# Kernel optimization log

Hardware: AMD Instinct MI355X
Metric: run time of the kernel (lower is better)

## Reference

```python
import jax, jax.numpy as jnp
import numpy as np

N = 8192
E = 262144
NFEAT = 200
NHID = 128
NOUT = 16
CLUSTERS = (10, 5)


def _layernorm(x, g, b, eps=1e-5):
    mu = jnp.mean(x, axis=-1, keepdims=True)
    var = jnp.var(x, axis=-1, keepdims=True)
    return (x - mu) / jnp.sqrt(var + eps) * g + b


def _gumbel_softmax_hard(logits, g, tau=1.0):
    # straight-through gumbel softmax (hard=True), dim=1
    y = jax.nn.softmax((logits + g) / tau, axis=1)
    hard = jax.nn.one_hot(jnp.argmax(y, axis=1), y.shape[1], dtype=y.dtype)
    return hard + y - jax.lax.stop_gradient(y)


def _row_normalize(x, eps=1e-12):
    n = jnp.linalg.norm(x, axis=1, keepdims=True)
    return x / jnp.maximum(n, eps)


def setup_inputs() -> dict:
    key = jax.random.key(0)
    ks = jax.random.split(key, 20)
    u0 = jax.random.uniform(ks[3], (N, CLUSTERS[0]), minval=1e-6, maxval=1.0 - 1e-6)
    u1 = jax.random.uniform(ks[4], (CLUSTERS[0], CLUSTERS[1]), minval=1e-6, maxval=1.0 - 1e-6)
    s = 0.05
    return {
        'x': jax.random.normal(ks[0], (N, NFEAT), dtype=jnp.float32),
        'edge_index': jax.random.randint(ks[1], (2, E), 0, N, dtype=jnp.int32),
        'edge_weight': jax.random.uniform(ks[2], (E,), dtype=jnp.float32),
        'gumbel0': -jnp.log(-jnp.log(u0)),
        'gumbel1': -jnp.log(-jnp.log(u1)),
        # GCN params (2 layers, layernorm)
        'Wg1': jax.random.normal(ks[5], (NHID, NFEAT)) * s,
        'bg1': jnp.zeros((NHID,)),
        'ln1_g': jnp.ones((NHID,)), 'ln1_b': jnp.zeros((NHID,)),
        'Wg2': jax.random.normal(ks[6], (NHID, NHID)) * s,
        'bg2': jnp.zeros((NHID,)),
        'ln2_g': jnp.ones((NHID,)), 'ln2_b': jnp.zeros((NHID,)),
        # per-level pool + encoder linears
        'pool0_W': jax.random.normal(ks[7], (CLUSTERS[0], NHID)) * s,
        'pool0_b': jnp.zeros((CLUSTERS[0],)),
        'pool1_W': jax.random.normal(ks[8], (CLUSTERS[1], NHID)) * s,
        'pool1_b': jnp.zeros((CLUSTERS[1],)),
        'enc0_W': jax.random.normal(ks[9], (NHID, NHID)) * s,
        'enc0_b': jnp.zeros((NHID,)),
        'enc1_W': jax.random.normal(ks[10], (NHID, NHID)) * s,
        'enc1_b': jnp.zeros((NHID,)),
        'fc_W': jax.random.normal(ks[11], (NOUT, 3 * NHID)) * s,
        'fc_b': jnp.zeros((NOUT,)),
    }


def reference(x, edge_index, edge_weight, gumbel0, gumbel1,
              Wg1, bg1, ln1_g, ln1_b, Wg2, bg2, ln2_g, ln2_b,
              pool0_W, pool0_b, pool1_W, pool1_b,
              enc0_W, enc0_b, enc1_W, enc1_b, fc_W, fc_b):
    src, dst = edge_index[0], edge_index[1]

    def agg(h):  # weighted neighbor sum: out[i] = sum_{e: dst_e=i} w_e * h[src_e]
        return jax.ops.segment_sum(h[src] * edge_weight[:, None], dst, num_segments=N)

    # bottom GCN encoder (2 layers, layernorm)
    h = agg(x) @ Wg1.T + bg1
    h = jax.nn.relu(_layernorm(h, ln1_g, ln1_b))
    h = agg(h) @ Wg2.T + bg2
    h = _layernorm(h, ln2_g, ln2_b)
    latent = jax.nn.relu(h)  # [N, nhid]
    all_latents = [latent]

    # dense adjacency (to_dense_adj)
    adj = jnp.zeros((N, N), dtype=x.dtype).at[src, dst].add(edge_weight)

    pools = [(pool0_W, pool0_b), (pool1_W, pool1_b)]
    encs = [(enc0_W, enc0_b), (enc1_W, enc1_b)]
    gumbels = [gumbel0, gumbel1]
    product = None
    for level in range(len(CLUSTERS)):
        pW, pb = pools[level]
        eW, eb = encs[level]
        assign = _gumbel_softmax_hard(latent @ pW.T + pb, gumbels[level])  # [n_l, K]
        product = assign if level == 0 else product @ assign  # [N, K]
        xc = _row_normalize(assign.T @ latent)  # [K, nhid]
        adj = assign.T @ adj @ assign  # [K, K]
        adj = adj / jnp.sum(adj + 1e-8)
        latent = jax.nn.relu((adj @ xc) @ eW.T + eb)  # [K, nhid]
        all_latents.append(product @ latent)  # [N, nhid]

    rep = jnp.concatenate(all_latents, axis=1)  # [N, 3*nhid]
    return rep @ fc_W.T + fc_b
```

## Files before the change

### kernel.cpp

```cpp
#include <hip/hip_runtime.h>

#define N_NODES 8192
#define N_EDGES 262144
#define NFEAT 200
#define NHID 128

template<int K>
__device__ __forceinline__ void gemm_body(const float* __restrict__ A,
                                          const float* __restrict__ W,
                                          float* __restrict__ C, int bid) {
    __shared__ float a_s[8 * K];
    int row0 = bid * 8;
    const float* Ab = A + (size_t)row0 * K;
    for (int idx = threadIdx.x; idx < 8 * K; idx += 128) a_s[idx] = Ab[idx];
    __syncthreads();
    int j = threadIdx.x;
    float acc[8] = {0.f, 0.f, 0.f, 0.f, 0.f, 0.f, 0.f, 0.f};
    const float4* W4 = (const float4*)(W + (size_t)j * K);
    for (int k4 = 0; k4 < K / 4; ++k4) {
        float4 w = W4[k4];
        int k = k4 * 4;
        #pragma unroll
        for (int r = 0; r < 8; ++r) {
            const float* ar = a_s + r * K + k;
            acc[r] += ar[0] * w.x + ar[1] * w.y + ar[2] * w.z + ar[3] * w.w;
        }
    }
    #pragma unroll
    for (int r = 0; r < 8; ++r) C[(size_t)(row0 + r) * 128 + j] = acc[r];
}

template<int K>
__global__ __launch_bounds__(128) void gemm_rows(const float* __restrict__ A,
                                                 const float* __restrict__ W,
                                                 float* __restrict__ C) {
    gemm_body<K>(A, W, C, blockIdx.x);
}

__global__ __launch_bounds__(128) void gemm1_hist(const float* __restrict__ A,
                                                  const float* __restrict__ W,
                                                  float* __restrict__ C,
                                                  const int* __restrict__ ei,
                                                  int* __restrict__ deg) {
    if (blockIdx.x < N_NODES / 8) {
        gemm_body<NFEAT>(A, W, C, blockIdx.x);
    } else {
        const int* dst = ei + N_EDGES;
        for (int e = (blockIdx.x - N_NODES / 8) * 128 + threadIdx.x; e < N_EDGES; e += 64 * 128)
            atomicAdd(&deg[dst[e]], 1);
    }
}

__global__ __launch_bounds__(256) void scan_kernel(const int* __restrict__ deg,
                                                   int* __restrict__ row_start,
                                                   int* __restrict__ cursor) {
    __shared__ int part[256];
    __shared__ int partx[257];
    int tid = threadIdx.x;
    int base = tid * 32;
    int s = 0;
    for (int i = 0; i < 32; ++i) s += deg[base + i];
    part[tid] = s;
    __syncthreads();
    if (tid == 0) {
        int run = 0;
        for (int i = 0; i < 256; ++i) { partx[i] = run; run += part[i]; }
        partx[256] = run;
    }
    __syncthreads();
    int run = partx[tid];
    for (int i = 0; i < 32; ++i) {
        row_start[base + i] = run;
        cursor[base + i] = run;
        run += deg[base + i];
    }
    if (tid == 255) row_start[N_NODES] = run;
}

__global__ __launch_bounds__(256) void scatter_kernel(const int* __restrict__ ei,
                                                      const float* __restrict__ ew,
                                                      int* __restrict__ cursor,
                                                      int2* __restrict__ esort, int E) {
    int e = blockIdx.x * blockDim.x + threadIdx.x;
    if (e < E) {
        int d = ei[E + e];
        int pos = atomicAdd(&cursor[d], 1);
        esort[pos] = make_int2(ei[e], __float_as_int(ew[e]));
    }
}

__global__ __launch_bounds__(256) void agg_ln_csr(const int* __restrict__ row_start,
                                                  const int2* __restrict__ esort,
                                                  const float* __restrict__ H,
                                                  float* __restrict__ out,
                                                  const float* __restrict__ bias,
                                                  const float* __restrict__ g,
                                                  const float* __restrict__ b) {
    int wave = (blockIdx.x * blockDim.x + threadIdx.x) >> 6;
    int lane = threadIdx.x & 63;
    int s0 = row_start[wave], s1 = row_start[wave + 1];
    float ax0 = 0.f, ay0 = 0.f, ax1 = 0.f, ay1 = 0.f;
    float ax2 = 0.f, ay2 = 0.f, ax3 = 0.f, ay3 = 0.f;
    int e = s0;
    for (; e + 3 < s1; e += 4) {
        int2 p0 = esort[e], p1 = esort[e + 1], p2 = esort[e + 2], p3 = esort[e + 3];
        float2 v0 = *(const float2*)(H + (size_t)p0.x * 128 + lane * 2);
        float2 v1 = *(const float2*)(H + (size_t)p1.x * 128 + lane * 2);
        float2 v2 = *(const float2*)(H + (size_t)p2.x * 128 + lane * 2);
        float2 v3 = *(const float2*)(H + (size_t)p3.x * 128 + lane * 2);
        float w0 = __int_as_float(p0.y), w1 = __int_as_float(p1.y);
        float w2 = __int_as_float(p2.y), w3 = __int_as_float(p3.y);
        ax0 += w0 * v0.x; ay0 += w0 * v0.y;
        ax1 += w1 * v1.x; ay1 += w1 * v1.y;
        ax2 += w2 * v2.x; ay2 += w2 * v2.y;
        ax3 += w3 * v3.x; ay3 += w3 * v3.y;
    }
    for (; e < s1; ++e) {
        int2 p0 = esort[e];
        float2 v0 = *(const float2*)(H + (size_t)p0.x * 128 + lane * 2);
        float w0 = __int_as_float(p0.y);
        ax0 += w0 * v0.x; ay0 += w0 * v0.y;
    }
    float2 bs = *(const float2*)(bias + lane * 2);
    float vx = (ax0 + ax1) + (ax2 + ax3) + bs.x;
    float vy = (ay0 + ay1) + (ay2 + ay3) + bs.y;
    float s = vx + vy;
    float ss = vx * vx + vy * vy;
    for (int off = 32; off; off >>= 1) {
        s += __shfl_xor(s, off, 64);
        ss += __shfl_xor(ss, off, 64);
    }
    float mu = s * (1.f / 128.f);
    float var = ss * (1.f / 128.f) - mu * mu;
    float rs = rsqrtf(var + 1e-5f);
    float2 gg = *(const float2*)(g + lane * 2);
    float2 bb = *(const float2*)(b + lane * 2);
    float y0 = fmaxf((vx - mu) * rs * gg.x + bb.x, 0.f);
    float y1 = fmaxf((vy - mu) * rs * gg.y + bb.y, 0.f);
    *(float2*)(out + (size_t)wave * 128 + lane * 2) = make_float2(y0, y1);
}

__global__ __launch_bounds__(256) void pool0_xc0(const float* __restrict__ latent,
                                                 const float* __restrict__ pW,
                                                 const float* __restrict__ pb,
                                                 const float* __restrict__ gum,
                                                 int* __restrict__ c0,
                                                 float* __restrict__ partials) {
    __shared__ float Ws[10 * 128];
    __shared__ float bs[10];
    __shared__ float acc[1280];
    for (int i = threadIdx.x; i < 1280; i += 256) { Ws[i] = pW[i]; acc[i] = 0.f; }
    if (threadIdx.x < 10) bs[threadIdx.x] = pb[threadIdx.x];
    __syncthreads();
    int lane = threadIdx.x & 63;
    int sub = lane & 7;
    int row = blockIdx.x * 32 + (threadIdx.x >> 6) * 8 + (lane >> 3);

    const float4* lp = (const float4*)(latent + (size_t)row * 128 + sub * 16);
    float4 x0 = lp[0], x1 = lp[1], x2 = lp[2], x3 = lp[3];
    float2 gj[5];
    #pragma unroll
    for (int j = 0; j < 5; ++j) gj[j] = *(const float2*)(gum + (size_t)row * 10 + j * 2);

    float p[10];
    #pragma unroll
    for (int k = 0; k < 10; ++k) {
        const float4* wk = (const float4*)(Ws + k * 128 + sub * 16);
        float4 w0 = wk[0], w1 = wk[1], w2 = wk[2], w3 = wk[3];
        float a = x0.x * w0.x + x0.y * w0.y + x0.z * w0.z + x0.w * w0.w;
        a += x1.x * w1.x + x1.y * w1.y + x1.z * w1.z + x1.w * w1.w;
        a += x2.x * w2.x + x2.y * w2.y + x2.z * w2.z + x2.w * w2.w;
        a += x3.x * w3.x + x3.y * w3.y + x3.z * w3.z + x3.w * w3.w;
        p[k] = a;
    }
    #pragma unroll
    for (int off = 1; off < 8; off <<= 1) {
        #pragma unroll
        for (int k = 0; k < 10; ++k) p[k] += __shfl_xor(p[k], off, 64);
    }
    int best = 0;
    float bv = p[0] + bs[0] + gj[0].x;
    #pragma unroll
    for (int k = 1; k < 10; ++k) {
        float gk = (k & 1) ? gj[k >> 1].y : gj[k >> 1].x;
        float z = p[k] + bs[k] + gk;
        if (z > bv) { bv = z; best = k; }
    }
    if (sub == 0) c0[row] = best;
    float* ap = acc + best * 128 + sub * 16;
    atomicAdd(ap + 0, x0.x);  atomicAdd(ap + 1, x0.y);
    atomicAdd(ap + 2, x0.z);  atomicAdd(ap + 3, x0.w);
    atomicAdd(ap + 4, x1.x);  atomicAdd(ap + 5, x1.y);
    atomicAdd(ap + 6, x1.z);  atomicAdd(ap + 7, x1.w);
    atomicAdd(ap + 8, x2.x);  atomicAdd(ap + 9, x2.y);
    atomicAdd(ap + 10, x2.z); atomicAdd(ap + 11, x2.w);
    atomicAdd(ap + 12, x3.x); atomicAdd(ap + 13, x3.y);
    atomicAdd(ap + 14, x3.z); atomicAdd(ap + 15, x3.w);
    __syncthreads();
    for (int i = threadIdx.x; i < 1280; i += 256)
        partials[(size_t)blockIdx.x * 1280 + i] = acc[i];
}

__global__ __launch_bounds__(256) void adj_xc0(const int* __restrict__ ei,
                                               const float* __restrict__ ew,
                                               const int* __restrict__ c0,
                                               float* __restrict__ A0,
                                               const float* __restrict__ partials,
                                               float* __restrict__ xc0, int E) {
    if (blockIdx.x < 256) {
        __shared__ float As[100];
        for (int i = threadIdx.x; i < 100; i += 256) As[i] = 0.f;
        __syncthreads();
        const int* src = ei;
        const int* dst = ei + E;
        for (int e = blockIdx.x * 256 + threadIdx.x; e < E; e += 256 * 256) {
            int a = c0[src[e]], b = c0[dst[e]];
            atomicAdd(&As[a * 10 + b], ew[e]);
        }
        __syncthreads();
        for (int i = threadIdx.x; i < 100; i += 256) atomicAdd(&A0[i], As[i]);
    } else {
        int k = blockIdx.x - 256;
        int d = threadIdx.x & 127;
        int half = threadIdx.x >> 7;
        int b0 = half * 128;
        float s0 = 0.f, s1 = 0.f, s2 = 0.f, s3 = 0.f;
        for (int b = b0; b < b0 + 128; b += 4) {
            s0 += partials[(size_t)(b    ) * 1280 + k * 128 + d];
            s1 += partials[(size_t)(b + 1) * 1280 + k * 128 + d];
            s2 += partials[(size_t)(b + 2) * 1280 + k * 128 + d];
            s3 += partials[(size_t)(b + 3) * 1280 + k * 128 + d];
        }
        __shared__ float sm[256];
        sm[threadIdx.x] = (s0 + s1) + (s2 + s3);
        __syncthreads();
        if (threadIdx.x < 128) xc0[k * 128 + d] = sm[threadIdx.x] + sm[threadIdx.x + 128];
    }
}

__global__ __launch_bounds__(256) void small_kernel(const float* __restrict__ xc0,
                                                    const float* __restrict__ A0,
                                                    const float* __restrict__ gum1,
                                                    const float* __restrict__ p1W,
                                                    const float* __restrict__ p1b,
                                                    const float* __restrict__ e0W,
                                                    const float* __restrict__ e0b,
                                                    const float* __restrict__ e1W,
                                                    const float* __restrict__ e1b,
                                                    const float* __restrict__ fcW,
                                                    const float* __restrict__ fcb,
                                                    float* __restrict__ tbl) {
    __shared__ float xc0n[10 * 128];
    __shared__ float adj0[100];
    __shared__ float m0[10 * 128];
    __shared__ float l1[10 * 128];
    __shared__ float xc1n[5 * 128];
    __shared__ float l2[5 * 128];
    __shared__ float A1[25];
    __shared__ int c1[10];
    __shared__ float red[4];

    int tid = threadIdx.x;
    int wid = tid >> 6, lane = tid & 63;

    for (int r = wid; r < 10; r += 4) {
        float2 v = *(const float2*)(xc0 + r * 128 + lane * 2);
        float ss = v.x * v.x + v.y * v.y;
        for (int off = 32; off; off >>= 1) ss += __shfl_xor(ss, off, 64);
        float sc = 1.f / fmaxf(sqrtf(ss), 1e-12f);
        xc0n[r * 128 + lane * 2] = v.x * sc;
        xc0n[r * 128 + lane * 2 + 1] = v.y * sc;
    }
    __syncthreads();
    if (tid == 0) {
        float s = 0.f;
        for (int i = 0; i < 100; ++i) s += A0[i];
        red[0] = s + 1e-6f;
    }
    __syncthreads();
    if (tid < 100) adj0[tid] = A0[tid] / red[0];
    __syncthreads();
    for (int idx = tid; idx < 1280; idx += 256) {
        int r = idx >> 7, d = idx & 127;
        float acc = 0.f;
        #pragma unroll
        for (int a = 0; a < 10; ++a) acc += adj0[r * 10 + a] * xc0n[a * 128 + d];
        m0[idx] = acc;
    }
    __syncthreads();
    for (int idx = tid; idx < 1280; idx += 256) {
        int r = idx >> 7, d = idx & 127;
        float acc = e0b[d];
        const float* wrow = e0W + d * 128;
        for (int k = 0; k < 128; ++k) acc += m0[r * 128 + k] * wrow[k];
        l1[idx] = fmaxf(acc, 0.f);
    }
    __syncthreads();
    if (tid < 10) {
        int best = 0;
        float bv = -1e30f;
        for (int j = 0; j < 5; ++j) {
            float acc = p1b[j] + gum1[tid * 5 + j];
            const float* wrow = p1W + j * 128;
            for (int k = 0; k < 128; ++k) acc += l1[tid * 128 + k] * wrow[k];
            if (acc > bv) { bv = acc; best = j; }
        }
        c1[tid] = best;
    }
    __syncthreads();
    for (int idx = tid; idx < 640; idx += 256) {
        int m = idx >> 7, d = idx & 127;
        float acc = 0.f;
        #pragma unroll
        for (int k = 0; k < 10; ++k)
            if (c1[k] == m) acc += l1[k * 128 + d];
        xc1n[idx] = acc;
    }
    __syncthreads();
    for (int r = wid; r < 5; r += 4) {
        float2 v = *(const float2*)(xc1n + r * 128 + lane * 2);
        float ss = v.x * v.x + v.y * v.y;
        for (int off = 32; off; off >>= 1) ss += __shfl_xor(ss, off, 64);
        float sc = 1.f / fmaxf(sqrtf(ss), 1e-12f);
        xc1n[r * 128 + lane * 2] = v.x * sc;
        xc1n[r * 128 + lane * 2 + 1] = v.y * sc;
    }
    __syncthreads();
    if (tid < 25) {
        int m = tid / 5, n = tid % 5;
        float acc = 0.f;
        for (int a = 0; a < 10; ++a)
            for (int b = 0; b < 10; ++b)
                if (c1[a] == m && c1[b] == n) acc += adj0[a * 10 + b];
        A1[tid] = acc;
    }
    __syncthreads();
    if (tid == 0) {
        float s = 0.f;
        for (int i = 0; i < 25; ++i) s += A1[i];
        red[1] = s + 25e-8f;
    }
    __syncthreads();
    float den1 = red[1];
    for (int idx = tid; idx < 640; idx += 256) {
        int r = idx >> 7, d = idx & 127;
        float acc = 0.f;
        #pragma unroll
        for (int a = 0; a < 5; ++a) acc += A1[r * 5 + a] * xc1n[a * 128 + d];
        m0[idx] = acc / den1;
    }
    __syncthreads();
    for (int idx = tid; idx < 640; idx += 256) {
        int r = idx >> 7, d = idx & 127;
        float acc = e1b[d];
        const float* wrow = e1W + d * 128;
        for (int k = 0; k < 128; ++k) acc += m0[r * 128 + k] * wrow[k];
        l2[idx] = fmaxf(acc, 0.f);
    }
    __syncthreads();
    for (int idx = tid; idx < 160; idx += 256) {
        int k = idx >> 4, o = idx & 15;
        float acc = fcb[o];
        const float* fB = fcW + o * 384 + 128;
        const float* fC = fcW + o * 384 + 256;
        const float* a1 = l1 + k * 128;
        const float* a2 = l2 + c1[k] * 128;
        for (int d = 0; d < 128; ++d) acc += a1[d] * fB[d] + a2[d] * fC[d];
        tbl[idx] = acc;
    }
}

__global__ __launch_bounds__(256) void out_kernel(const float* __restrict__ latent,
                                                  const int* __restrict__ c0,
                                                  const float* __restrict__ tbl,
                                                  const float* __restrict__ fcW,
                                                  float* __restrict__ out) {
    __shared__ float fA[16 * 128];
    __shared__ float ts[160];
    for (int i = threadIdx.x; i < 2048; i += 256) {
        int o = i >> 7, d = i & 127;
        fA[i] = fcW[o * 384 + d];
    }
    for (int i = threadIdx.x; i < 160; i += 256) ts[i] = tbl[i];
    __syncthreads();
    int lane = threadIdx.x & 63;
    int sub = lane & 7;
    int row = blockIdx.x * 32 + (threadIdx.x >> 6) * 8 + (lane >> 3);
    const float4* lp = (const float4*)(latent + (size_t)row * 128 + sub * 16);
    float4 x0 = lp[0], x1 = lp[1], x2 = lp[2], x3 = lp[3];
    float p[16];
    #pragma unroll
    for (int o = 0; o < 16; ++o) {
        const float4* fo = (const float4*)(fA + o * 128 + sub * 16);
        float4 w0 = fo[0], w1 = fo[1], w2 = fo[2], w3 = fo[3];
        float a = x0.x * w0.x + x0.y * w0.y + x0.z * w0.z + x0.w * w0.w;
        a += x1.x * w1.x + x1.y * w1.y + x1.z * w1.z + x1.w * w1.w;
        a += x2.x * w2.x + x2.y * w2.y + x2.z * w2.z + x2.w * w2.w;
        a += x3.x * w3.x + x3.y * w3.y + x3.z * w3.z + x3.w * w3.w;
        p[o] = a;
    }
    #pragma unroll
    for (int off = 1; off < 8; off <<= 1) {
        #pragma unroll
        for (int o = 0; o < 16; ++o) p[o] += __shfl_xor(p[o], off, 64);
    }
    int c = c0[row];
    float2 r = make_float2(p[2 * sub] + ts[c * 16 + 2 * sub],
                           p[2 * sub + 1] + ts[c * 16 + 2 * sub + 1]);
    *(float2*)(out + (size_t)row * 16 + 2 * sub) = r;
}

extern "C" void kernel_launch(void* const* d_in, const int* in_sizes, int n_in,
                              void* d_out, int out_size, void* d_ws, size_t ws_size,
                              hipStream_t stream) {
    const float* x    = (const float*)d_in[0];
    const int*   ei   = (const int*)d_in[1];
    const float* ew   = (const float*)d_in[2];
    const float* g0   = (const float*)d_in[3];
    const float* g1   = (const float*)d_in[4];
    const float* Wg1  = (const float*)d_in[5];
    const float* bg1  = (const float*)d_in[6];
    const float* ln1g = (const float*)d_in[7];
    const float* ln1b = (const float*)d_in[8];
    const float* Wg2  = (const float*)d_in[9];
    const float* bg2  = (const float*)d_in[10];
    const float* ln2g = (const float*)d_in[11];
    const float* ln2b = (const float*)d_in[12];
    const float* p0W  = (const float*)d_in[13];
    const float* p0b  = (const float*)d_in[14];
    const float* p1W  = (const float*)d_in[15];
    const float* p1b  = (const float*)d_in[16];
    const float* e0W  = (const float*)d_in[17];
    const float* e0b  = (const float*)d_in[18];
    const float* e1W  = (const float*)d_in[19];
    const float* e1b  = (const float*)d_in[20];
    const float* fcW  = (const float*)d_in[21];
    const float* fcb  = (const float*)d_in[22];
    float* out = (float*)d_out;

    float* ws   = (float*)d_ws;
    float* bufA = ws;
    float* bufB = bufA + (size_t)N_NODES * 128;
    int*   c0   = (int*)(bufB + (size_t)N_NODES * 128);
    float* xc0  = (float*)(c0 + N_NODES);
    float* tbl  = xc0 + 1280;
    int*   deg  = (int*)(tbl + 160);
    float* A0   = (float*)(deg + N_NODES);
    int*   row_start = (int*)(A0 + 100);
    int*   cursor    = row_start + N_NODES + 2;
    int2*  esort     = (int2*)(cursor + N_NODES);
    float* partials  = bufA;

    hipMemsetAsync(deg, 0, (N_NODES + 100) * sizeof(int), stream);

    gemm1_hist<<<N_NODES / 8 + 64, 128, 0, stream>>>(x, Wg1, bufA, ei, deg);
    scan_kernel<<<1, 256, 0, stream>>>(deg, row_start, cursor);
    scatter_kernel<<<N_EDGES / 256, 256, 0, stream>>>(ei, ew, cursor, esort, N_EDGES);
    agg_ln_csr<<<N_NODES / 4, 256, 0, stream>>>(row_start, esort, bufA, bufB,
                                                bg1, ln1g, ln1b);

    gemm_rows<NHID><<<N_NODES / 8, 128, 0, stream>>>(bufB, Wg2, bufA);
    agg_ln_csr<<<N_NODES / 4, 256, 0, stream>>>(row_start, esort, bufA, bufB,
                                                bg2, ln2g, ln2b);

    pool0_xc0<<<256, 256, 0, stream>>>(bufB, p0W, p0b, g0, c0, partials);
    adj_xc0<<<266, 256, 0, stream>>>(ei, ew, c0, A0, partials, xc0, N_EDGES);

    small_kernel<<<1, 256, 0, stream>>>(xc0, A0, g1, p1W, p1b, e0W, e0b, e1W, e1b,
                                        fcW, fcb, tbl);

    out_kernel<<<256, 256, 0, stream>>>(bufB, c0, tbl, fcW, out);
}
```

Baseline: 181.3 us.

## Fuse CSR aggregation with GEMM2 and with pool0 assignment

Merges the first layer's aggregation and layernorm with the Wg2 GEMM in one kernel, staging four normalized rows in shared memory. It also merges the second aggregation and layernorm with the pool0 cluster assignment and per-cluster partial sums. This removes two kernel launches and the global write and re-read of the intermediate activations. In exchange, each output row of the fused GEMM reloads Wg2 rows per block of four, and the partials reduction now covers 512 blocks instead of 256.

```diff
diff --git a/kernel.cpp b/kernel.cpp
--- a/kernel.cpp
+++ b/kernel.cpp
@@ -28,13 +28,6 @@
     }
     #pragma unroll
     for (int r = 0; r < 8; ++r) C[(size_t)(row0 + r) * 128 + j] = acc[r];
-}
-
-template<int K>
-__global__ __launch_bounds__(128) void gemm_rows(const float* __restrict__ A,
-                                                 const float* __restrict__ W,
-                                                 float* __restrict__ C) {
-    gemm_body<K>(A, W, C, blockIdx.x);
 }
 
 __global__ __launch_bounds__(128) void gemm1_hist(const float* __restrict__ A,
@@ -89,16 +82,11 @@
     }
 }
 
-__global__ __launch_bounds__(256) void agg_ln_csr(const int* __restrict__ row_start,
-                                                  const int2* __restrict__ esort,
-                                                  const float* __restrict__ H,
-                                                  float* __restrict__ out,
-                                                  const float* __restrict__ bias,
-                                                  const float* __restrict__ g,
-                                                  const float* __restrict__ b) {
-    int wave = (blockIdx.x * blockDim.x + threadIdx.x) >> 6;
-    int lane = threadIdx.x & 63;
-    int s0 = row_start[wave], s1 = row_start[wave + 1];
+__device__ __forceinline__ float2 csr_gather(const int* __restrict__ row_start,
+                                             const int2* __restrict__ esort,
+                                             const float* __restrict__ H,
+                                             int row, int lane) {
+    int s0 = row_start[row], s1 = row_start[row + 1];
     float ax0 = 0.f, ay0 = 0.f, ax1 = 0.f, ay1 = 0.f;
     float ax2 = 0.f, ay2 = 0.f, ax3 = 0.f, ay3 = 0.f;
     int e = s0;
@@ -121,11 +109,16 @@
         float w0 = __int_as_float(p0.y);
         ax0 += w0 * v0.x; ay0 += w0 * v0.y;
     }
+    return make_float2((ax0 + ax1) + (ax2 + ax3), (ay0 + ay1) + (ay2 + ay3));
+}
+
+__device__ __forceinline__ float2 ln_relu(float vx, float vy, int lane,
+                                          const float* __restrict__ bias,
+                                          const float* __restrict__ g,
+                                          const float* __restrict__ b) {
     float2 bs = *(const float2*)(bias + lane * 2);
-    float vx = (ax0 + ax1) + (ax2 + ax3) + bs.x;
-    float vy = (ay0 + ay1) + (ay2 + ay3) + bs.y;
-    float s = vx + vy;
-    float ss = vx * vx + vy * vy;
+    vx += bs.x; vy += bs.y;
+    float s = vx + vy, ss = vx * vx + vy * vy;
     for (int off = 32; off; off >>= 1) {
         s += __shfl_xor(s, off, 64);
         ss += __shfl_xor(ss, off, 64);
@@ -135,70 +128,92 @@
     float rs = rsqrtf(var + 1e-5f);
     float2 gg = *(const float2*)(g + lane * 2);
     float2 bb = *(const float2*)(b + lane * 2);
-    float y0 = fmaxf((vx - mu) * rs * gg.x + bb.x, 0.f);
-    float y1 = fmaxf((vy - mu) * rs * gg.y + bb.y, 0.f);
-    *(float2*)(out + (size_t)wave * 128 + lane * 2) = make_float2(y0, y1);
-}
-
-__global__ __launch_bounds__(256) void pool0_xc0(const float* __restrict__ latent,
-                                                 const float* __restrict__ pW,
-                                                 const float* __restrict__ pb,
-                                                 const float* __restrict__ gum,
-                                                 int* __restrict__ c0,
-                                                 float* __restrict__ partials) {
-    __shared__ float Ws[10 * 128];
-    __shared__ float bs[10];
-    __shared__ float acc[1280];
-    for (int i = threadIdx.x; i < 1280; i += 256) { Ws[i] = pW[i]; acc[i] = 0.f; }
-    if (threadIdx.x < 10) bs[threadIdx.x] = pb[threadIdx.x];
-    __syncthreads();
-    int lane = threadIdx.x & 63;
-    int sub = lane & 7;
-    int row = blockIdx.x * 32 + (threadIdx.x >> 6) * 8 + (lane >> 3);
-
-    const float4* lp = (const float4*)(latent + (size_t)row * 128 + sub * 16);
-    float4 x0 = lp[0], x1 = lp[1], x2 = lp[2], x3 = lp[3];
-    float2 gj[5];
-    #pragma unroll
-    for (int j = 0; j < 5; ++j) gj[j] = *(const float2*)(gum + (size_t)row * 10 + j * 2);
-
-    float p[10];
-    #pragma unroll
-    for (int k = 0; k < 10; ++k) {
-        const float4* wk = (const float4*)(Ws + k * 128 + sub * 16);
-        float4 w0 = wk[0], w1 = wk[1], w2 = wk[2], w3 = wk[3];
-        float a = x0.x * w0.x + x0.y * w0.y + x0.z * w0.z + x0.w * w0.w;
-        a += x1.x * w1.x + x1.y * w1.y + x1.z * w1.z + x1.w * w1.w;
-        a += x2.x * w2.x + x2.y * w2.y + x2.z * w2.z + x2.w * w2.w;
-        a += x3.x * w3.x + x3.y * w3.y + x3.z * w3.z + x3.w * w3.w;
-        p[k] = a;
-    }
-    #pragma unroll
-    for (int off = 1; off < 8; off <<= 1) {
-        #pragma unroll
-        for (int k = 0; k < 10; ++k) p[k] += __shfl_xor(p[k], off, 64);
-    }
-    int best = 0;
-    float bv = p[0] + bs[0] + gj[0].x;
-    #pragma unroll
-    for (int k = 1; k < 10; ++k) {
-        float gk = (k & 1) ? gj[k >> 1].y : gj[k >> 1].x;
-        float z = p[k] + bs[k] + gk;
-        if (z > bv) { bv = z; best = k; }
-    }
-    if (sub == 0) c0[row] = best;
-    float* ap = acc + best * 128 + sub * 16;
-    atomicAdd(ap + 0, x0.x);  atomicAdd(ap + 1, x0.y);
-    atomicAdd(ap + 2, x0.z);  atomicAdd(ap + 3, x0.w);
-    atomicAdd(ap + 4, x1.x);  atomicAdd(ap + 5, x1.y);
-    atomicAdd(ap + 6, x1.z);  atomicAdd(ap + 7, x1.w);
-    atomicAdd(ap + 8, x2.x);  atomicAdd(ap + 9, x2.y);
-    atomicAdd(ap + 10, x2.z); atomicAdd(ap + 11, x2.w);
-    atomicAdd(ap + 12, x3.x); atomicAdd(ap + 13, x3.y);
-    atomicAdd(ap + 14, x3.z); atomicAdd(ap + 15, x3.w);
+    return make_float2(fmaxf((vx - mu) * rs * gg.x + bb.x, 0.f),
+                       fmaxf((vy - mu) * rs * gg.y + bb.y, 0.f));
+}
+
+__global__ __launch_bounds__(256) void agg1_gemm2(const int* __restrict__ row_start,
+                                                  const int2* __restrict__ esort,
+                                                  const float* __restrict__ bufA,
+                                                  const float* __restrict__ Wg2,
+                                                  float* __restrict__ bufC,
+                                                  const float* __restrict__ bias,
+                                                  const float* __restrict__ g,
+                                                  const float* __restrict__ b) {
+    __shared__ float rows[4 * 128];
+    int lane = threadIdx.x & 63, wid = threadIdx.x >> 6;
+    int row0 = blockIdx.x * 4;
+    {
+        float2 a = csr_gather(row_start, esort, bufA, row0 + wid, lane);
+        float2 y = ln_relu(a.x, a.y, lane, bias, g, b);
+        rows[wid * 128 + lane * 2] = y.x;
+        rows[wid * 128 + lane * 2 + 1] = y.y;
+    }
+    __syncthreads();
+    int j = threadIdx.x & 127, rh = threadIdx.x >> 7;
+    const float4* wp = (const float4*)(Wg2 + (size_t)j * 128);
+    const float4* r0 = (const float4*)(rows + rh * 128);
+    const float4* r1 = (const float4*)(rows + (rh + 2) * 128);
+    float acc0 = 0.f, acc1 = 0.f;
+    #pragma unroll 8
+    for (int kk = 0; kk < 32; ++kk) {
+        float4 w = wp[kk];
+        float4 a0 = r0[kk], a1 = r1[kk];
+        acc0 += a0.x * w.x + a0.y * w.y + a0.z * w.z + a0.w * w.w;
+        acc1 += a1.x * w.x + a1.y * w.y + a1.z * w.z + a1.w * w.w;
+    }
+    bufC[(size_t)(row0 + rh) * 128 + j] = acc0;
+    bufC[(size_t)(row0 + rh + 2) * 128 + j] = acc1;
+}
+
+__global__ __launch_bounds__(256) void agg2_pool0(const int* __restrict__ row_start,
+                                                  const int2* __restrict__ esort,
+                                                  const float* __restrict__ bufC,
+                                                  float* __restrict__ latent,
+                                                  const float* __restrict__ bias,
+                                                  const float* __restrict__ g,
+                                                  const float* __restrict__ b,
+                                                  const float* __restrict__ p0W,
+                                                  const float* __restrict__ p0b,
+                                                  const float* __restrict__ gum,
+                                                  int* __restrict__ c0,
+                                                  float* __restrict__ partials) {
+    __shared__ float Ws[1280];
+    __shared__ float accs[1280];
+    __shared__ float bsh[10];
+    for (int i = threadIdx.x; i < 1280; i += 256) { Ws[i] = p0W[i]; accs[i] = 0.f; }
+    if (threadIdx.x < 10) bsh[threadIdx.x] = p0b[threadIdx.x];
+    __syncthreads();
+    int lane = threadIdx.x & 63, wid = threadIdx.x >> 6;
+    int base = blockIdx.x * 16;
+    for (int rr = 0; rr < 4; ++rr) {
+        int row = base + rr * 4 + wid;
+        float2 a = csr_gather(row_start, esort, bufC, row, lane);
+        float2 y = ln_relu(a.x, a.y, lane, bias, g, b);
+        *(float2*)(latent + (size_t)row * 128 + lane * 2) = y;
+        float pk[10];
+        #pragma unroll
+        for (int k = 0; k < 10; ++k)
+            pk[k] = y.x * Ws[k * 128 + lane * 2] + y.y * Ws[k * 128 + lane * 2 + 1];
+        for (int off = 32; off; off >>= 1) {
+            #pragma unroll
+            for (int k = 0; k < 10; ++k) pk[k] += __shfl_xor(pk[k], off, 64);
+        }
+        const float* gr = gum + (size_t)row * 10;
+        int best = 0;
+        float bv = pk[0] + bsh[0] + gr[0];
+        #pragma unroll
+        for (int k = 1; k < 10; ++k) {
+            float z = pk[k] + bsh[k] + gr[k];
+            if (z > bv) { bv = z; best = k; }
+        }
+        if (lane == 0) c0[row] = best;
+        atomicAdd(&accs[best * 128 + lane * 2], y.x);
+        atomicAdd(&accs[best * 128 + lane * 2 + 1], y.y);
+    }
     __syncthreads();
     for (int i = threadIdx.x; i < 1280; i += 256)
-        partials[(size_t)blockIdx.x * 1280 + i] = acc[i];
+        partials[(size_t)blockIdx.x * 1280 + i] = accs[i];
 }
 
 __global__ __launch_bounds__(256) void adj_xc0(const int* __restrict__ ei,
@@ -211,21 +226,17 @@
         __shared__ float As[100];
         for (int i = threadIdx.x; i < 100; i += 256) As[i] = 0.f;
         __syncthreads();
-        const int* src = ei;
-        const int* dst = ei + E;
         for (int e = blockIdx.x * 256 + threadIdx.x; e < E; e += 256 * 256) {
-            int a = c0[src[e]], b = c0[dst[e]];
+            int a = c0[ei[e]], b = c0[ei[E + e]];
             atomicAdd(&As[a * 10 + b], ew[e]);
         }
         __syncthreads();
         for (int i = threadIdx.x; i < 100; i += 256) atomicAdd(&A0[i], As[i]);
     } else {
         int k = blockIdx.x - 256;
-        int d = threadIdx.x & 127;
-        int half = threadIdx.x >> 7;
-        int b0 = half * 128;
+        int d = threadIdx.x & 127, half = threadIdx.x >> 7;
         float s0 = 0.f, s1 = 0.f, s2 = 0.f, s3 = 0.f;
-        for (int b = b0; b < b0 + 128; b += 4) {
+        for (int b = half * 256; b < half * 256 + 256; b += 4) {
             s0 += partials[(size_t)(b    ) * 1280 + k * 128 + d];
             s1 += partials[(size_t)(b + 1) * 1280 + k * 128 + d];
             s2 += partials[(size_t)(b + 2) * 1280 + k * 128 + d];
@@ -441,7 +452,8 @@
     float* ws   = (float*)d_ws;
     float* bufA = ws;
     float* bufB = bufA + (size_t)N_NODES * 128;
-    int*   c0   = (int*)(bufB + (size_t)N_NODES * 128);
+    float* bufC = bufB + (size_t)N_NODES * 128;
+    int*   c0   = (int*)(bufC + (size_t)N_NODES * 128);
     float* xc0  = (float*)(c0 + N_NODES);
     float* tbl  = xc0 + 1280;
     int*   deg  = (int*)(tbl + 160);
@@ -456,14 +468,13 @@
     gemm1_hist<<<N_NODES / 8 + 64, 128, 0, stream>>>(x, Wg1, bufA, ei, deg);
     scan_kernel<<<1, 256, 0, stream>>>(deg, row_start, cursor);
     scatter_kernel<<<N_EDGES / 256, 256, 0, stream>>>(ei, ew, cursor, esort, N_EDGES);
-    agg_ln_csr<<<N_NODES / 4, 256, 0, stream>>>(row_start, esort, bufA, bufB,
+
+    agg1_gemm2<<<N_NODES / 4, 256, 0, stream>>>(row_start, esort, bufA, Wg2, bufC,
                                                 bg1, ln1g, ln1b);
 
-    gemm_rows<NHID><<<N_NODES / 8, 128, 0, stream>>>(bufB, Wg2, bufA);
-    agg_ln_csr<<<N_NODES / 4, 256, 0, stream>>>(row_start, esort, bufA, bufB,
-                                                bg2, ln2g, ln2b);
-
-    pool0_xc0<<<256, 256, 0, stream>>>(bufB, p0W, p0b, g0, c0, partials);
+    agg2_pool0<<<512, 256, 0, stream>>>(row_start, esort, bufC, bufB,
+                                        bg2, ln2g, ln2b, p0W, p0b, g0, c0, partials);
+
     adj_xc0<<<266, 256, 0, stream>>>(ei, ew, c0, A0, partials, xc0, N_EDGES);
 
     small_kernel<<<1, 256, 0, stream>>>(xc0, A0, g1, p1W, p1b, e0W, e0b, e1W, e1b,
```

Measured after the change: 207.9 us. +14.7%, slower.
